# Kernel optimization log

Hardware: AMD Instinct MI355X
Metric: run time of the kernel (lower is better)

The kernel has to match this reference:

```python
import jax, jax.numpy as jnp
import numpy as np

NODE_LIST = [4, 5, 5]
NODE_NUM = 100  # prod(NODE_LIST)


def _attn(q, k, v):
    # stand-in for the external (auto/cross) correlation layer:
    # scaled dot-product attention over the sequence axis, [B,L,C]x[B,S,C]->[B,L,C]
    C = q.shape[-1]
    scores = jnp.einsum('blc,bsc->bls', q, k) / jnp.sqrt(jnp.asarray(C, q.dtype))
    w = jax.nn.softmax(scores, axis=-1)
    return jnp.einsum('bls,bsc->blc', w, v)


def setup_inputs() -> dict:
    key = jax.random.key(0)
    k1, k2 = jax.random.split(key)
    x = jax.random.normal(k1, (400, 96, 512), dtype=jnp.float32)
    cross = jax.random.normal(k2, (400, 96, 512), dtype=jnp.float32)
    return {"x": x, "cross": cross}


def reference(x, cross):
    B, L, C = x.shape
    S = cross.shape[1]
    Bb = B // NODE_NUM
    n = len(NODE_LIST)

    # leaf-level correlation (dropout is identity in eval)
    x_leaf = _attn(x, cross, cross)

    x_exp = x.reshape([Bb] + NODE_LIST + [L, C])
    c_exp = cross.reshape([Bb] + NODE_LIST + [S, C])

    levels = []
    for i in range(n):
        keep = int(np.prod(NODE_LIST[: i + 1]))
        reduce_node = int(np.prod(NODE_LIST[i + 1:]))
        xt = x_exp.reshape([Bb * keep] + NODE_LIST[i + 1:] + [L, C])
        ct = c_exp.reshape([Bb * keep] + NODE_LIST[i + 1:] + [S, C])
        # hierarchical gather-mean-pool over the finer levels
        for _ in range(n - i - 1):
            xt = xt.mean(axis=1)
            ct = ct.mean(axis=1)
        o = _attn(xt, ct, ct)  # [Bb*keep, L, C]
        # scatter back: repeat over the reduced sub-nodes
        o = jnp.broadcast_to(o[:, None, :, :], (Bb * keep, reduce_node, L, C))
        levels.append(o.reshape([Bb] + NODE_LIST + [L, C]))

    x_inter = jnp.mean(jnp.stack(levels, axis=0), axis=0).reshape(B, L, C)
    return x_leaf + x_inter
```

## Files before the change

### kernel.cpp

```cpp
#include <hip/hip_runtime.h>

#define LROW  96
#define CDIM  512
#define LC    (LROW*CDIM)

#define KC_LD 136
#define S_LD  97
#define P_LD  104
#define VT_LD 104
#define REGA  26112
#define REGB  37248
#define LDSZ  (REGA + REGB)

typedef __bf16 bf16;
typedef bf16  bf16x2 __attribute__((ext_vector_type(2)));
typedef bf16  bf16x8 __attribute__((ext_vector_type(8)));
typedef float f32x4  __attribute__((ext_vector_type(4)));

#define MFMA16(a,b,c) __builtin_amdgcn_mfma_f32_16x16x32_bf16((a),(b),(c),0,0,0)

__device__ __forceinline__ bf16x8 cvt8(f32x4 a, f32x4 b) {
    bf16x8 v;
    v[0]=(bf16)a.x; v[1]=(bf16)a.y; v[2]=(bf16)a.z; v[3]=(bf16)a.w;
    v[4]=(bf16)b.x; v[5]=(bf16)b.y; v[6]=(bf16)b.z; v[7]=(bf16)b.w;
    return v;
}

template<bool HASADD>
__device__ __forceinline__ void attn_core(
    const float* __restrict__ q, const float* __restrict__ kv,
    float outScale,
    const float* __restrict__ add0, const float* __restrict__ add1,
    float* __restrict__ out, char* lds)
{
    const int tid  = threadIdx.x;
    const int wave = tid >> 6;
    const int lane = tid & 63;
    const int l16  = lane & 15;
    const int quad = lane >> 4;
    const int srow = tid >> 2;
    const int spart = tid & 3;

    bf16*  Kc   = (bf16*)lds;
    bf16*  P    = (bf16*)lds;
    float* Smat = (float*)(lds + REGA);
    bf16*  Vt   = (bf16*)(lds + REGA);

    f32x4 acc[6];
#pragma unroll
    for (int i = 0; i < 6; i++) acc[i] = {0.f, 0.f, 0.f, 0.f};

    const float* kvst = kv + srow*CDIM + spart*32;
    const float* qrow = q + (wave*16 + l16)*CDIM + quad*8;

    f32x4 sbuf[8], qbuf[8];
#pragma unroll
    for (int i = 0; i < 8; i++) sbuf[i] = *(const f32x4*)(kvst + i*4);
#pragma unroll
    for (int ks = 0; ks < 4; ks++) {
        qbuf[2*ks]   = *(const f32x4*)(qrow + ks*32);
        qbuf[2*ks+1] = *(const f32x4*)(qrow + ks*32 + 4);
    }

#pragma unroll
    for (int c = 0; c < 4; c++) {
        bf16x8 af[4];
#pragma unroll
        for (int ks = 0; ks < 4; ks++) af[ks] = cvt8(qbuf[2*ks], qbuf[2*ks+1]);
        bf16* kdst = Kc + srow*KC_LD + spart*32;
#pragma unroll
        for (int i = 0; i < 4; i++)
            *(bf16x8*)(kdst + i*8) = cvt8(sbuf[2*i], sbuf[2*i+1]);
        if (c < 3) {
            const int cb = (c+1)*128;
#pragma unroll
            for (int i = 0; i < 8; i++) sbuf[i] = *(const f32x4*)(kvst + cb + i*4);
#pragma unroll
            for (int ks = 0; ks < 4; ks++) {
                qbuf[2*ks]   = *(const f32x4*)(qrow + cb + ks*32);
                qbuf[2*ks+1] = *(const f32x4*)(qrow + cb + ks*32 + 4);
            }
        }
        __syncthreads();
#pragma unroll
        for (int ks = 0; ks < 4; ks++) {
#pragma unroll
            for (int ct = 0; ct < 6; ct++) {
                bf16x8 bk = *(const bf16x8*)(Kc + (ct*16 + l16)*KC_LD + ks*32 + quad*8);
                acc[ct] = MFMA16(af[ks], bk, acc[ct]);
            }
        }
        __syncthreads();
    }

    const float rs = 0.04419417382415922f;
#pragma unroll
    for (int ct = 0; ct < 6; ct++)
#pragma unroll
        for (int r = 0; r < 4; r++)
            Smat[(wave*16 + quad*4 + r)*S_LD + ct*16 + l16] = acc[ct][r] * rs;

    const int rp = tid % 48;
    const int cg = tid / 48;
    const float* v0 = kv + (2*rp)*CDIM + cg*16;
    const float* v1 = v0 + CDIM;
    f32x4 vbuf[8];
#pragma unroll
    for (int i = 0; i < 4; i++) {
        vbuf[i]   = *(const f32x4*)(v0 + i*4);
        vbuf[4+i] = *(const f32x4*)(v1 + i*4);
    }
    __syncthreads();

    {
        const float* Srow = Smat + srow*S_LD + spart*24;
        float mx = -1e30f;
#pragma unroll
        for (int j = 0; j < 24; j++) mx = fmaxf(mx, Srow[j]);
        mx = fmaxf(mx, __shfl_xor(mx, 1));
        mx = fmaxf(mx, __shfl_xor(mx, 2));
        float e[24], sum = 0.f;
#pragma unroll
        for (int j = 0; j < 24; j++) { e[j] = __expf(Srow[j] - mx); sum += e[j]; }
        sum += __shfl_xor(sum, 1);
        sum += __shfl_xor(sum, 2);
        const float inv = 1.f / sum;
        bf16* Prow = P + srow*P_LD + spart*24;
#pragma unroll
        for (int j = 0; j < 24; j++) Prow[j] = (bf16)(e[j] * inv);
    }
    __syncthreads();

#pragma unroll
    for (int nb = 0; nb < 4; nb++) {
        bf16* vdst = Vt + cg*16*VT_LD + 2*rp;
#pragma unroll
        for (int j = 0; j < 16; j++) {
            float f0 = vbuf[j >> 2][j & 3];
            float f1 = vbuf[4 + (j >> 2)][j & 3];
            bf16x2 pr; pr[0] = (bf16)f0; pr[1] = (bf16)f1;
            *(bf16x2*)(vdst + j*VT_LD) = pr;
        }
        if (nb < 3) {
            const int cb = (nb+1)*128;
#pragma unroll
            for (int i = 0; i < 4; i++) {
                vbuf[i]   = *(const f32x4*)(v0 + cb + i*4);
                vbuf[4+i] = *(const f32x4*)(v1 + cb + i*4);
            }
        }
        __syncthreads();

        f32x4 oacc[8];
#pragma unroll
        for (int i = 0; i < 8; i++) oacc[i] = {0.f, 0.f, 0.f, 0.f};
#pragma unroll
        for (int sb = 0; sb < 96; sb += 32) {
            bf16x8 ap = *(const bf16x8*)(P + (wave*16 + l16)*P_LD + sb + quad*8);
#pragma unroll
            for (int ct = 0; ct < 8; ct++) {
                bf16x8 bv = *(const bf16x8*)(Vt + (ct*16 + l16)*VT_LD + sb + quad*8);
                oacc[ct] = MFMA16(ap, bv, oacc[ct]);
            }
        }
        __syncthreads();

        const int orow0 = wave*16 + quad*4;
#pragma unroll
        for (int ct = 0; ct < 8; ct++) {
            const int col = nb*128 + ct*16 + l16;
#pragma unroll
            for (int r = 0; r < 4; r++) {
                const int idx = (orow0 + r)*CDIM + col;
                float v = oacc[ct][r] * outScale;
                if (HASADD) v += add0[idx] + add1[idx];
                out[idx] = v;
            }
        }
    }
}

__global__ __launch_bounds__(256) void means_kernel(
    const float* __restrict__ x, const float* __restrict__ cr,
    float* __restrict__ m1x, float* __restrict__ m1c,
    float* __restrict__ m0x, float* __restrict__ m0c)
{
    const int idx = blockIdx.x*256 + threadIdx.x;
    const int g  = idx / LC;
    const int lc = idx - g*LC;
    const float* xb = x  + (size_t)(g*25)*LC + lc;
    const float* cb = cr + (size_t)(g*25)*LC + lc;
    float ax = 0.f, ac = 0.f;
#pragma unroll
    for (int qq = 0; qq < 5; qq++) {
        float sx = 0.f, sc = 0.f;
#pragma unroll
        for (int j = 0; j < 5; j++) {
            sx += xb[(size_t)(qq*5 + j)*LC];
            sc += cb[(size_t)(qq*5 + j)*LC];
        }
        m1x[(size_t)(g*5 + qq)*LC + lc] = sx * 0.2f;
        m1c[(size_t)(g*5 + qq)*LC + lc] = sc * 0.2f;
        ax += sx; ac += sc;
    }
    m0x[(size_t)g*LC + lc] = ax * 0.04f;
    m0c[(size_t)g*LC + lc] = ac * 0.04f;
}

__global__ __launch_bounds__(384, 3) void attn_levels_kernel(
    const float* __restrict__ m1x, const float* __restrict__ m1c,
    const float* __restrict__ m0x, const float* __restrict__ m0c,
    float* __restrict__ lvl1s, float* __restrict__ lvl0s)
{
    __shared__ char lds[LDSZ];
    const int j = blockIdx.x;
    const float *q, *kv; float* o;
    if (j < 80) { q = m1x + (size_t)j*LC; kv = m1c + (size_t)j*LC; o = lvl1s + (size_t)j*LC; }
    else { const int g = j - 80; q = m0x + (size_t)g*LC; kv = m0c + (size_t)g*LC; o = lvl0s + (size_t)g*LC; }
    attn_core<false>(q, kv, 1.f/3.f, nullptr, nullptr, o, lds);
}

__global__ __launch_bounds__(384, 3) void attn_full_kernel(
    const float* __restrict__ x, const float* __restrict__ cr,
    const float* __restrict__ lvl0s, const float* __restrict__ lvl1s,
    float* __restrict__ out)
{
    __shared__ char lds[LDSZ];
    const int b = blockIdx.x;
    attn_core<true>(x + (size_t)b*LC, cr + (size_t)b*LC, 4.f/3.f,
                    lvl0s + (size_t)(b/25)*LC, lvl1s + (size_t)(b/5)*LC,
                    out + (size_t)b*LC, lds);
}

extern "C" void kernel_launch(void* const* d_in, const int* in_sizes, int n_in,
                              void* d_out, int out_size, void* d_ws, size_t ws_size,
                              hipStream_t stream)
{
    const float* x  = (const float*)d_in[0];
    const float* cr = (const float*)d_in[1];
    float* out = (float*)d_out;
    float* ws  = (float*)d_ws;

    float* m1x   = ws;
    float* m1c   = m1x   + (size_t)80*LC;
    float* m0x   = m1c   + (size_t)80*LC;
    float* m0c   = m0x   + (size_t)16*LC;
    float* lvl1s = m0c   + (size_t)16*LC;
    float* lvl0s = lvl1s + (size_t)80*LC;

    means_kernel<<<dim3((16*LC)/256), dim3(256), 0, stream>>>(x, cr, m1x, m1c, m0x, m0c);
    attn_levels_kernel<<<dim3(96), dim3(384), 0, stream>>>(m1x, m1c, m0x, m0c, lvl1s, lvl0s);
    attn_full_kernel<<<dim3(400), dim3(384), 0, stream>>>(x, cr, lvl0s, lvl1s, out);
}
```

Baseline: 295.7 us.

## Store intermediates in bf16 and pre-convert inputs during means pass

Means, per-level attention outputs, and (when workspace allows) full bf16 copies of x and cross are written as bf16. The means kernel emits the bf16 copies while it already reads the inputs, so the full attention kernel loads half the bytes and skips in-kernel conversion. This adds an extra write of 2x400x96x512 bf16 values plus a reread, trading extra traffic in the means pass for less traffic in the attention passes. Level outputs added to the result are also rounded to bf16, which slightly reduces accuracy.

```diff
diff --git a/kernel.cpp b/kernel.cpp
--- a/kernel.cpp
+++ b/kernel.cpp
@@ -25,13 +25,20 @@
     v[4]=(bf16)b.x; v[5]=(bf16)b.y; v[6]=(bf16)b.z; v[7]=(bf16)b.w;
     return v;
 }
-
-template<bool HASADD>
+__device__ __forceinline__ bf16x8 load8(const float* p) {
+    f32x4 a = *(const f32x4*)p, b = *(const f32x4*)(p + 4);
+    return cvt8(a, b);
+}
+__device__ __forceinline__ bf16x8 load8(const bf16* p) {
+    return *(const bf16x8*)p;
+}
+
+template<bool FULL, typename TIN>
 __device__ __forceinline__ void attn_core(
-    const float* __restrict__ q, const float* __restrict__ kv,
+    const TIN* __restrict__ q, const TIN* __restrict__ kv,
     float outScale,
-    const float* __restrict__ add0, const float* __restrict__ add1,
-    float* __restrict__ out, char* lds)
+    const bf16* __restrict__ add0, const bf16* __restrict__ add1,
+    void* __restrict__ outp, char* lds)
 {
     const int tid  = threadIdx.x;
     const int wave = tid >> 6;
@@ -50,36 +57,29 @@
 #pragma unroll
     for (int i = 0; i < 6; i++) acc[i] = {0.f, 0.f, 0.f, 0.f};
 
-    const float* kvst = kv + srow*CDIM + spart*32;
-    const float* qrow = q + (wave*16 + l16)*CDIM + quad*8;
-
-    f32x4 sbuf[8], qbuf[8];
-#pragma unroll
-    for (int i = 0; i < 8; i++) sbuf[i] = *(const f32x4*)(kvst + i*4);
-#pragma unroll
-    for (int ks = 0; ks < 4; ks++) {
-        qbuf[2*ks]   = *(const f32x4*)(qrow + ks*32);
-        qbuf[2*ks+1] = *(const f32x4*)(qrow + ks*32 + 4);
-    }
+    const TIN* kvst = kv + srow*CDIM + spart*32;
+    const TIN* qrow = q + (wave*16 + l16)*CDIM + quad*8;
+
+    bf16x8 kbuf[4], qbuf[4];
+#pragma unroll
+    for (int i = 0; i < 4; i++) kbuf[i] = load8(kvst + i*8);
+#pragma unroll
+    for (int ks = 0; ks < 4; ks++) qbuf[ks] = load8(qrow + ks*32);
 
 #pragma unroll
     for (int c = 0; c < 4; c++) {
         bf16x8 af[4];
 #pragma unroll
-        for (int ks = 0; ks < 4; ks++) af[ks] = cvt8(qbuf[2*ks], qbuf[2*ks+1]);
+        for (int ks = 0; ks < 4; ks++) af[ks] = qbuf[ks];
         bf16* kdst = Kc + srow*KC_LD + spart*32;
 #pragma unroll
-        for (int i = 0; i < 4; i++)
-            *(bf16x8*)(kdst + i*8) = cvt8(sbuf[2*i], sbuf[2*i+1]);
+        for (int i = 0; i < 4; i++) *(bf16x8*)(kdst + i*8) = kbuf[i];
         if (c < 3) {
             const int cb = (c+1)*128;
 #pragma unroll
-            for (int i = 0; i < 8; i++) sbuf[i] = *(const f32x4*)(kvst + cb + i*4);
-#pragma unroll
-            for (int ks = 0; ks < 4; ks++) {
-                qbuf[2*ks]   = *(const f32x4*)(qrow + cb + ks*32);
-                qbuf[2*ks+1] = *(const f32x4*)(qrow + cb + ks*32 + 4);
-            }
+            for (int i = 0; i < 4; i++) kbuf[i] = load8(kvst + cb + i*8);
+#pragma unroll
+            for (int ks = 0; ks < 4; ks++) qbuf[ks] = load8(qrow + cb + ks*32);
         }
         __syncthreads();
 #pragma unroll
@@ -102,14 +102,10 @@
 
     const int rp = tid % 48;
     const int cg = tid / 48;
-    const float* v0 = kv + (2*rp)*CDIM + cg*16;
-    const float* v1 = v0 + CDIM;
-    f32x4 vbuf[8];
-#pragma unroll
-    for (int i = 0; i < 4; i++) {
-        vbuf[i]   = *(const f32x4*)(v0 + i*4);
-        vbuf[4+i] = *(const f32x4*)(v1 + i*4);
-    }
+    const TIN* v0 = kv + (2*rp)*CDIM + cg*16;
+    bf16x8 vbuf[4];
+    vbuf[0] = load8(v0);          vbuf[1] = load8(v0 + 8);
+    vbuf[2] = load8(v0 + CDIM);   vbuf[3] = load8(v0 + CDIM + 8);
     __syncthreads();
 
     {
@@ -136,18 +132,15 @@
         bf16* vdst = Vt + cg*16*VT_LD + 2*rp;
 #pragma unroll
         for (int j = 0; j < 16; j++) {
-            float f0 = vbuf[j >> 2][j & 3];
-            float f1 = vbuf[4 + (j >> 2)][j & 3];
-            bf16x2 pr; pr[0] = (bf16)f0; pr[1] = (bf16)f1;
+            bf16x2 pr;
+            pr[0] = vbuf[j >> 3][j & 7];
+            pr[1] = vbuf[2 + (j >> 3)][j & 7];
             *(bf16x2*)(vdst + j*VT_LD) = pr;
         }
         if (nb < 3) {
             const int cb = (nb+1)*128;
-#pragma unroll
-            for (int i = 0; i < 4; i++) {
-                vbuf[i]   = *(const f32x4*)(v0 + cb + i*4);
-                vbuf[4+i] = *(const f32x4*)(v1 + cb + i*4);
-            }
+            vbuf[0] = load8(v0 + cb);        vbuf[1] = load8(v0 + cb + 8);
+            vbuf[2] = load8(v0 + cb + CDIM); vbuf[3] = load8(v0 + cb + CDIM + 8);
         }
         __syncthreads();
 
@@ -173,63 +166,75 @@
             for (int r = 0; r < 4; r++) {
                 const int idx = (orow0 + r)*CDIM + col;
                 float v = oacc[ct][r] * outScale;
-                if (HASADD) v += add0[idx] + add1[idx];
-                out[idx] = v;
-            }
-        }
-    }
-}
-
+                if constexpr (FULL) {
+                    v += (float)add0[idx] + (float)add1[idx];
+                    ((float*)outp)[idx] = v;
+                } else {
+                    ((bf16*)outp)[idx] = (bf16)v;
+                }
+            }
+        }
+    }
+}
+
+template<bool COPY>
 __global__ __launch_bounds__(256) void means_kernel(
     const float* __restrict__ x, const float* __restrict__ cr,
-    float* __restrict__ m1x, float* __restrict__ m1c,
-    float* __restrict__ m0x, float* __restrict__ m0c)
+    bf16* __restrict__ m1x, bf16* __restrict__ m1c,
+    bf16* __restrict__ m0x, bf16* __restrict__ m0c,
+    bf16* __restrict__ xb, bf16* __restrict__ cb)
 {
     const int idx = blockIdx.x*256 + threadIdx.x;
     const int g  = idx / LC;
     const int lc = idx - g*LC;
-    const float* xb = x  + (size_t)(g*25)*LC + lc;
-    const float* cb = cr + (size_t)(g*25)*LC + lc;
+    const float* xp = x  + (size_t)(g*25)*LC + lc;
+    const float* cp = cr + (size_t)(g*25)*LC + lc;
     float ax = 0.f, ac = 0.f;
 #pragma unroll
     for (int qq = 0; qq < 5; qq++) {
         float sx = 0.f, sc = 0.f;
 #pragma unroll
         for (int j = 0; j < 5; j++) {
-            sx += xb[(size_t)(qq*5 + j)*LC];
-            sc += cb[(size_t)(qq*5 + j)*LC];
-        }
-        m1x[(size_t)(g*5 + qq)*LC + lc] = sx * 0.2f;
-        m1c[(size_t)(g*5 + qq)*LC + lc] = sc * 0.2f;
+            const size_t b = (size_t)(qq*5 + j)*LC;
+            float xv = xp[b], cv = cp[b];
+            if (COPY) {
+                xb[(size_t)(g*25 + qq*5 + j)*LC + lc] = (bf16)xv;
+                cb[(size_t)(g*25 + qq*5 + j)*LC + lc] = (bf16)cv;
+            }
+            sx += xv; sc += cv;
+        }
+        m1x[(size_t)(g*5 + qq)*LC + lc] = (bf16)(sx * 0.2f);
+        m1c[(size_t)(g*5 + qq)*LC + lc] = (bf16)(sc * 0.2f);
         ax += sx; ac += sc;
     }
-    m0x[(size_t)g*LC + lc] = ax * 0.04f;
-    m0c[(size_t)g*LC + lc] = ac * 0.04f;
+    m0x[(size_t)g*LC + lc] = (bf16)(ax * 0.04f);
+    m0c[(size_t)g*LC + lc] = (bf16)(ac * 0.04f);
 }
 
 __global__ __launch_bounds__(384, 3) void attn_levels_kernel(
-    const float* __restrict__ m1x, const float* __restrict__ m1c,
-    const float* __restrict__ m0x, const float* __restrict__ m0c,
-    float* __restrict__ lvl1s, float* __restrict__ lvl0s)
+    const bf16* __restrict__ m1x, const bf16* __restrict__ m1c,
+    const bf16* __restrict__ m0x, const bf16* __restrict__ m0c,
+    bf16* __restrict__ lvl1s, bf16* __restrict__ lvl0s)
 {
     __shared__ char lds[LDSZ];
     const int j = blockIdx.x;
-    const float *q, *kv; float* o;
+    const bf16 *q, *kv; bf16* o;
     if (j < 80) { q = m1x + (size_t)j*LC; kv = m1c + (size_t)j*LC; o = lvl1s + (size_t)j*LC; }
     else { const int g = j - 80; q = m0x + (size_t)g*LC; kv = m0c + (size_t)g*LC; o = lvl0s + (size_t)g*LC; }
-    attn_core<false>(q, kv, 1.f/3.f, nullptr, nullptr, o, lds);
-}
-
+    attn_core<false, bf16>(q, kv, 1.f/3.f, nullptr, nullptr, o, lds);
+}
+
+template<typename TIN>
 __global__ __launch_bounds__(384, 3) void attn_full_kernel(
-    const float* __restrict__ x, const float* __restrict__ cr,
-    const float* __restrict__ lvl0s, const float* __restrict__ lvl1s,
+    const TIN* __restrict__ x, const TIN* __restrict__ cr,
+    const bf16* __restrict__ lvl0s, const bf16* __restrict__ lvl1s,
     float* __restrict__ out)
 {
     __shared__ char lds[LDSZ];
     const int b = blockIdx.x;
-    attn_core<true>(x + (size_t)b*LC, cr + (size_t)b*LC, 4.f/3.f,
-                    lvl0s + (size_t)(b/25)*LC, lvl1s + (size_t)(b/5)*LC,
-                    out + (size_t)b*LC, lds);
+    attn_core<true, TIN>(x + (size_t)b*LC, cr + (size_t)b*LC, 4.f/3.f,
+                         lvl0s + (size_t)(b/25)*LC, lvl1s + (size_t)(b/5)*LC,
+                         out + (size_t)b*LC, lds);
 }
 
 extern "C" void kernel_launch(void* const* d_in, const int* in_sizes, int n_in,
@@ -239,16 +244,33 @@
     const float* x  = (const float*)d_in[0];
     const float* cr = (const float*)d_in[1];
     float* out = (float*)d_out;
-    float* ws  = (float*)d_ws;
-
-    float* m1x   = ws;
-    float* m1c   = m1x   + (size_t)80*LC;
-    float* m0x   = m1c   + (size_t)80*LC;
-    float* m0c   = m0x   + (size_t)16*LC;
-    float* lvl1s = m0c   + (size_t)16*LC;
-    float* lvl0s = lvl1s + (size_t)80*LC;
-
-    means_kernel<<<dim3((16*LC)/256), dim3(256), 0, stream>>>(x, cr, m1x, m1c, m0x, m0c);
-    attn_levels_kernel<<<dim3(96), dim3(384), 0, stream>>>(m1x, m1c, m0x, m0c, lvl1s, lvl0s);
-    attn_full_kernel<<<dim3(400), dim3(384), 0, stream>>>(x, cr, lvl0s, lvl1s, out);
-}
+    bf16* ws = (bf16*)d_ws;
+
+    bf16* m1x   = ws;
+    bf16* m1c   = m1x   + (size_t)80*LC;
+    bf16* m0x   = m1c   + (size_t)80*LC;
+    bf16* m0c   = m0x   + (size_t)16*LC;
+    bf16* lvl1s = m0c   + (size_t)16*LC;
+    bf16* lvl0s = lvl1s + (size_t)80*LC;
+    bf16* xb    = lvl0s + (size_t)16*LC;
+    bf16* cb    = xb    + (size_t)400*LC;
+
+    const size_t need = (size_t)1088 * LC * sizeof(bf16);
+    const bool copy = ws_size >= need;
+
+    if (copy) {
+        means_kernel<true><<<dim3((16*LC)/256), dim3(256), 0, stream>>>(
+            x, cr, m1x, m1c, m0x, m0c, xb, cb);
+        attn_levels_kernel<<<dim3(96), dim3(384), 0, stream>>>(
+            m1x, m1c, m0x, m0c, lvl1s, lvl0s);
+        attn_full_kernel<bf16><<<dim3(400), dim3(384), 0, stream>>>(
+            xb, cb, lvl0s, lvl1s, out);
+    } else {
+        means_kernel<false><<<dim3((16*LC)/256), dim3(256), 0, stream>>>(
+            x, cr, m1x, m1c, m0x, m0c, nullptr, nullptr);
+        attn_levels_kernel<<<dim3(96), dim3(384), 0, stream>>>(
+            m1x, m1c, m0x, m0c, lvl1s, lvl0s);
+        attn_full_kernel<float><<<dim3(400), dim3(384), 0, stream>>>(
+            x, cr, lvl0s, lvl1s, out);
+    }
+}
```

New measurement: 260.6 us. 11.9% less time.
